# Kernel optimization log

Measured on AMD Instinct MI355X. Metric: run time of the kernel, lower is better.

The kernel has to match this reference:

```python
import jax, jax.numpy as jnp
import numpy as np

B, T, S, E, H = 4, 1024, 1024, 768, 12
D = E // H  # head_dim = 64
SCALE = D ** -0.5


def setup_inputs() -> dict:
    key = jax.random.key(0)
    ks = jax.random.split(key, 12)
    w = lambda k: jax.random.normal(k, (E, E), jnp.float32) * 0.02
    b = lambda k: jax.random.normal(k, (E,), jnp.float32) * 0.02
    return {
        "hidden_states": jax.random.normal(ks[0], (B, T, E), jnp.float32),
        "key_value_states": jax.random.normal(ks[1], (B, S, E), jnp.float32),
        "position_bias": jax.random.normal(ks[2], (T, S, D), jnp.float32),
        "Wq": w(ks[3]), "bq": b(ks[4]),
        "Wk": w(ks[5]), "bk": b(ks[6]),
        "Wv": w(ks[7]), "bv": b(ks[8]),
        "Wo": w(ks[9]), "bo": b(ks[10]),
    }


def _heads(x, L):
    # [B, L, E] -> [B, H, L, D]
    return x.reshape(B, L, H, D).transpose(0, 2, 1, 3)


def reference(hidden_states, key_value_states, position_bias,
              Wq, bq, Wk, bk, Wv, bv, Wo, bo):
    # projections (torch Linear: x @ W.T + b); query pre-scaled like original
    q = _heads((hidden_states @ Wq.T + bq) * SCALE, T)   # [B,H,T,D]
    k = _heads(key_value_states @ Wk.T + bk, S)           # [B,H,S,D]
    v = _heads(key_value_states @ Wv.T + bv, S)           # [B,H,S,D]

    # QK^T plus relative position bias (reshape_q @ position_bias^T in torch)
    scores = jnp.einsum('bhtd,bhsd->bhts', q, k)
    scores = scores + jnp.einsum('bhtd,tsd->bhts', q, position_bias)

    probs = jax.nn.softmax(scores, axis=-1)               # [B,H,T,S]
    out = jnp.einsum('bhts,bhsd->bhtd', probs, v)          # [B,H,T,D]
    out = out.transpose(0, 2, 1, 3).reshape(B, T, E)       # [B,T,E]
    return out @ Wo.T + bo
```

## Files before the change

### kernel.cpp

```cpp
#include <hip/hip_runtime.h>
#include <hip/hip_bf16.h>

#define BB 4
#define TT 1024
#define SS 1024
#define EE 768
#define HH 12
#define DD 64
#define BH (BB*HH)
#define QSCALE 0.125f

typedef __attribute__((ext_vector_type(8))) short bf16x8;
typedef __attribute__((ext_vector_type(4))) float f32x4;

__device__ __forceinline__ unsigned short bf16_rne(float x) {
    unsigned u = __builtin_bit_cast(unsigned, x);
    u += 0x7FFFu + ((u >> 16) & 1u);
    return (unsigned short)(u >> 16);
}
__device__ __forceinline__ void split_bf16(float x, unsigned short& h, unsigned short& l) {
    unsigned u = __builtin_bit_cast(unsigned, x);
    unsigned r = u + 0x7FFFu + ((u >> 16) & 1u);
    h = (unsigned short)(r >> 16);
    const float fh = __builtin_bit_cast(float, r & 0xFFFF0000u);
    l = bf16_rne(x - fh);
}

template<int HEAD_LAYOUT>
__global__ __launch_bounds__(256) void gemm_xwt_mfma(
    const float* __restrict__ X, const float* __restrict__ W,
    const float* __restrict__ bias, float* __restrict__ out, float scale)
{
    __shared__ __align__(16) unsigned short Ah[128][40], Al[128][40];
    __shared__ __align__(16) unsigned short Bh[64][40],  Bl[64][40];

    const int bm = blockIdx.x * 128, bn = blockIdx.y * 64;
    const int tid  = threadIdx.x;
    const int wave = tid >> 6, lane = tid & 63;
    const int wr = (wave >> 1) * 64;
    const int wc = (wave & 1) * 32;
    const int lr = lane & 15;
    const int lg = lane >> 4;

    f32x4 acc[4][2];
    #pragma unroll
    for (int mi = 0; mi < 4; ++mi)
        #pragma unroll
        for (int nj = 0; nj < 2; ++nj) acc[mi][nj] = (f32x4){0.f, 0.f, 0.f, 0.f};

    for (int k0 = 0; k0 < 768; k0 += 32) {
        #pragma unroll
        for (int i = 0; i < 4; ++i) {
            const int f = i * 256 + tid, r = f >> 3, c = (f & 7) * 4;
            const float4 v = *(const float4*)&X[(size_t)(bm + r) * 768 + k0 + c];
            unsigned short h0,h1,h2,h3,l0,l1,l2,l3;
            split_bf16(v.x, h0, l0); split_bf16(v.y, h1, l1);
            split_bf16(v.z, h2, l2); split_bf16(v.w, h3, l3);
            *(ushort4*)&Ah[r][c] = make_ushort4(h0, h1, h2, h3);
            *(ushort4*)&Al[r][c] = make_ushort4(l0, l1, l2, l3);
        }
        #pragma unroll
        for (int i = 0; i < 2; ++i) {
            const int f = i * 256 + tid, r = f >> 3, c = (f & 7) * 4;
            const float4 v = *(const float4*)&W[(size_t)(bn + r) * 768 + k0 + c];
            unsigned short h0,h1,h2,h3,l0,l1,l2,l3;
            split_bf16(v.x, h0, l0); split_bf16(v.y, h1, l1);
            split_bf16(v.z, h2, l2); split_bf16(v.w, h3, l3);
            *(ushort4*)&Bh[r][c] = make_ushort4(h0, h1, h2, h3);
            *(ushort4*)&Bl[r][c] = make_ushort4(l0, l1, l2, l3);
        }
        __syncthreads();

        bf16x8 ah[4], al[4], bh[2], bl[2];
        #pragma unroll
        for (int mi = 0; mi < 4; ++mi) {
            ah[mi] = *(const bf16x8*)&Ah[wr + mi * 16 + lr][lg * 8];
            al[mi] = *(const bf16x8*)&Al[wr + mi * 16 + lr][lg * 8];
        }
        #pragma unroll
        for (int nj = 0; nj < 2; ++nj) {
            bh[nj] = *(const bf16x8*)&Bh[wc + nj * 16 + lr][lg * 8];
            bl[nj] = *(const bf16x8*)&Bl[wc + nj * 16 + lr][lg * 8];
        }
        #pragma unroll
        for (int mi = 0; mi < 4; ++mi)
            #pragma unroll
            for (int nj = 0; nj < 2; ++nj) {
                acc[mi][nj] = __builtin_amdgcn_mfma_f32_16x16x32_bf16(ah[mi], bl[nj], acc[mi][nj], 0, 0, 0);
                acc[mi][nj] = __builtin_amdgcn_mfma_f32_16x16x32_bf16(al[mi], bh[nj], acc[mi][nj], 0, 0, 0);
                acc[mi][nj] = __builtin_amdgcn_mfma_f32_16x16x32_bf16(ah[mi], bh[nj], acc[mi][nj], 0, 0, 0);
            }
        __syncthreads();
    }

    #pragma unroll
    for (int mi = 0; mi < 4; ++mi) {
        #pragma unroll
        for (int nj = 0; nj < 2; ++nj) {
            const int gn = bn + wc + nj * 16 + lr;
            #pragma unroll
            for (int r = 0; r < 4; ++r) {
                const int gm = bm + wr + mi * 16 + lg * 4 + r;
                const float val = (acc[mi][nj][r] + bias[gn]) * scale;
                if (HEAD_LAYOUT) {
                    const int b = gm >> 10, l = gm & 1023;
                    const int h = gn >> 6,  d = gn & 63;
                    out[(size_t)((b * HH + h) * 1024 + l) * 64 + d] = val;
                } else {
                    out[(size_t)gm * 768 + gn] = val;
                }
            }
        }
    }
}

__global__ __launch_bounds__(192) void bias_fill(
    const float* __restrict__ q, const float* __restrict__ pos,
    float* __restrict__ biasbuf)
{
    const int t  = blockIdx.x;
    const int sc = blockIdx.y;
    __shared__ float Qs[64][49];
    __shared__ float Ps[64][129];
    const int tid = threadIdx.x;

    for (int f = tid; f < 768; f += 192) {
        const int bh = f >> 4, d4 = (f & 15) * 4;
        const float4 w = *(const float4*)&q[(size_t)(bh * 1024 + t) * 64 + d4];
        Qs[d4 + 0][bh] = w.x; Qs[d4 + 1][bh] = w.y;
        Qs[d4 + 2][bh] = w.z; Qs[d4 + 3][bh] = w.w;
    }
    for (int f = tid; f < 2048; f += 192) {
        const int sl = f >> 4, d4 = (f & 15) * 4;
        const float4 w = *(const float4*)&pos[((size_t)t * 1024 + sc * 128 + sl) * 64 + d4];
        Ps[d4 + 0][sl] = w.x; Ps[d4 + 1][sl] = w.y;
        Ps[d4 + 2][sl] = w.z; Ps[d4 + 3][sl] = w.w;
    }
    __syncthreads();

    const int sg = tid & 31;
    const int g  = tid >> 5;
    float acc[8][4];
    #pragma unroll
    for (int i = 0; i < 8; ++i)
        #pragma unroll
        for (int u = 0; u < 4; ++u) acc[i][u] = 0.f;

    #pragma unroll 4
    for (int d = 0; d < 64; ++d) {
        float p[4], qv[8];
        #pragma unroll
        for (int u = 0; u < 4; ++u) p[u] = Ps[d][sg + 32 * u];
        #pragma unroll
        for (int i = 0; i < 8; ++i) qv[i] = Qs[d][g * 8 + i];
        #pragma unroll
        for (int i = 0; i < 8; ++i)
            #pragma unroll
            for (int u = 0; u < 4; ++u) acc[i][u] += qv[i] * p[u];
    }
    #pragma unroll
    for (int i = 0; i < 8; ++i) {
        const int bh = g * 8 + i;
        #pragma unroll
        for (int u = 0; u < 4; ++u) {
            const int s = sc * 128 + sg + 32 * u;
            biasbuf[((size_t)bh * 1024 + t) * 1024 + s] = acc[i][u];
        }
    }
}

__global__ __launch_bounds__(256) void flash_attn(
    const float* __restrict__ q, const float* __restrict__ k,
    const float* __restrict__ v, const float* __restrict__ biasbuf,
    float* __restrict__ attn)
{
    const int mt = blockIdx.x;
    const int bh = blockIdx.y;
    const int b = bh / HH, h = bh % HH;
    const int tid = threadIdx.x;
    const int tx = tid & 15;
    const int ty = tid >> 4;

    __shared__ float4 Qs4[64][17];
    __shared__ float4 KP4[64][17];
    __shared__ float  Vt[64][68];

    for (int f = tid; f < 1024; f += 256) {
        const int r = f >> 4, c4 = f & 15;
        Qs4[r][c4] = *(const float4*)&q[((size_t)bh * 1024 + mt * 64 + r) * 64 + c4 * 4];
    }

    float o[4][4];
    float mrow[4], lrow[4];
    #pragma unroll
    for (int i = 0; i < 4; ++i) {
        mrow[i] = -1e30f; lrow[i] = 0.f;
        #pragma unroll
        for (int j = 0; j < 4; ++j) o[i][j] = 0.f;
    }

    for (int s0 = 0; s0 < 1024; s0 += 64) {
        float bias_r[4][4];
        #pragma unroll
        for (int i = 0; i < 4; ++i) {
            const size_t row = ((size_t)bh * 1024 + mt * 64 + ty + 16 * i) * 1024;
            #pragma unroll
            for (int j = 0; j < 4; ++j)
                bias_r[i][j] = biasbuf[row + s0 + tx + 16 * j];
        }

        __syncthreads();
        for (int f = tid; f < 1024; f += 256) {
            const int r = f >> 4, c4 = f & 15;
            KP4[r][c4] = *(const float4*)&k[((size_t)bh * 1024 + s0 + r) * 64 + c4 * 4];
        }
        for (int f = tid; f < 1024; f += 256) {
            const int r = f & 63, c4 = f >> 6;
            const float4 w = *(const float4*)&v[((size_t)bh * 1024 + s0 + r) * 64 + c4 * 4];
            Vt[c4 * 4 + 0][r] = w.x; Vt[c4 * 4 + 1][r] = w.y;
            Vt[c4 * 4 + 2][r] = w.z; Vt[c4 * 4 + 3][r] = w.w;
        }
        __syncthreads();

        float accs[4][4];
        #pragma unroll
        for (int i = 0; i < 4; ++i)
            #pragma unroll
            for (int j = 0; j < 4; ++j) accs[i][j] = bias_r[i][j];
        #pragma unroll
        for (int k4 = 0; k4 < 16; ++k4) {
            float4 a4[4], b4[4];
            #pragma unroll
            for (int i = 0; i < 4; ++i) a4[i] = Qs4[ty + 16 * i][k4];
            #pragma unroll
            for (int j = 0; j < 4; ++j) b4[j] = KP4[tx + 16 * j][k4];
            #pragma unroll
            for (int i = 0; i < 4; ++i)
                #pragma unroll
                for (int j = 0; j < 4; ++j)
                    accs[i][j] += a4[i].x * b4[j].x + a4[i].y * b4[j].y
                                + a4[i].z * b4[j].z + a4[i].w * b4[j].w;
        }

        float p[4][4];
        #pragma unroll
        for (int i = 0; i < 4; ++i) {
            float tmax = fmaxf(fmaxf(accs[i][0], accs[i][1]),
                               fmaxf(accs[i][2], accs[i][3]));
            #pragma unroll
            for (int off = 8; off > 0; off >>= 1)
                tmax = fmaxf(tmax, __shfl_xor(tmax, off, 16));
            const float newm = fmaxf(mrow[i], tmax);
            const float scale = __expf(mrow[i] - newm);
            float psum = 0.f;
            #pragma unroll
            for (int j = 0; j < 4; ++j) {
                p[i][j] = __expf(accs[i][j] - newm);
                psum += p[i][j];
            }
            #pragma unroll
            for (int off = 8; off > 0; off >>= 1)
                psum += __shfl_xor(psum, off, 16);
            lrow[i] = lrow[i] * scale + psum;
            mrow[i] = newm;
            #pragma unroll
            for (int j = 0; j < 4; ++j) o[i][j] *= scale;
        }

        __syncthreads();
        {
            float* Pf = (float*)KP4;
            #pragma unroll
            for (int i = 0; i < 4; ++i)
                #pragma unroll
                for (int j = 0; j < 4; ++j)
                    Pf[(ty + 16 * i) * 68 + tx + 16 * j] = p[i][j];
        }
        __syncthreads();

        {
            const float* Pf = (const float*)KP4;
            #pragma unroll 4
            for (int sk4 = 0; sk4 < 16; ++sk4) {
                float4 p4[4], v4[4];
                #pragma unroll
                for (int i = 0; i < 4; ++i)
                    p4[i] = *(const float4*)&Pf[(ty + 16 * i) * 68 + sk4 * 4];
                #pragma unroll
                for (int j = 0; j < 4; ++j)
                    v4[j] = *(const float4*)&Vt[tx + 16 * j][sk4 * 4];
                #pragma unroll
                for (int i = 0; i < 4; ++i)
                    #pragma unroll
                    for (int j = 0; j < 4; ++j)
                        o[i][j] += p4[i].x * v4[j].x + p4[i].y * v4[j].y
                                 + p4[i].z * v4[j].z + p4[i].w * v4[j].w;
            }
        }
    }

    #pragma unroll
    for (int i = 0; i < 4; ++i) {
        const int t = mt * 64 + ty + 16 * i;
        const float inv = 1.0f / lrow[i];
        #pragma unroll
        for (int j = 0; j < 4; ++j) {
            const int d = tx + 16 * j;
            attn[((size_t)b * 1024 + t) * 768 + h * 64 + d] = o[i][j] * inv;
        }
    }
}

extern "C" void kernel_launch(void* const* d_in, const int* in_sizes, int n_in,
                              void* d_out, int out_size, void* d_ws, size_t ws_size,
                              hipStream_t stream)
{
    const float* hidden = (const float*)d_in[0];
    const float* kv     = (const float*)d_in[1];
    const float* pos    = (const float*)d_in[2];
    const float* Wq = (const float*)d_in[3];  const float* bq = (const float*)d_in[4];
    const float* Wk = (const float*)d_in[5];  const float* bk = (const float*)d_in[6];
    const float* Wv = (const float*)d_in[7];  const float* bv = (const float*)d_in[8];
    const float* Wo = (const float*)d_in[9];  const float* bo = (const float*)d_in[10];
    float* out = (float*)d_out;

    float* q       = (float*)d_ws;
    float* kbuf    = q     + (size_t)BH * 1024 * 64;
    float* vbuf    = kbuf  + (size_t)BH * 1024 * 64;
    float* attn    = vbuf  + (size_t)BH * 1024 * 64;
    float* biasbuf = attn  + (size_t)BB * 1024 * EE;

    const dim3 gproj(32, 12), blk(256);
    gemm_xwt_mfma<1><<<gproj, blk, 0, stream>>>(hidden, Wq, bq, q,    QSCALE);
    gemm_xwt_mfma<1><<<gproj, blk, 0, stream>>>(kv,     Wk, bk, kbuf, 1.0f);
    gemm_xwt_mfma<1><<<gproj, blk, 0, stream>>>(kv,     Wv, bv, vbuf, 1.0f);

    bias_fill <<<dim3(1024, 8), 192, 0, stream>>>(q, pos, biasbuf);
    flash_attn<<<dim3(16, 48),  256, 0, stream>>>(q, kbuf, vbuf, biasbuf, attn);

    gemm_xwt_mfma<0><<<gproj, blk, 0, stream>>>(attn, Wo, bo, out, 1.0f);
}
```

Measured before the change: 912.7 us.

## Port flash attention to bf16 MFMA with split-precision QK and block swizzle

Rewrites the attention kernel so QK^T and PV run on MFMA 16x16x32 bf16 instructions instead of scalar FP32 FMAs. QK^T keeps near-FP32 accuracy by splitting Q and K into high and low bf16 parts and issuing three MFMAs, while P and V are rounded to plain bf16. Bias tiles are staged through shared memory with coalesced loads, and block IDs are remapped across a 1D grid to change scheduling and cache locality. The cost is lower precision in the PV product and extra conversion work when staging K and V.

```diff
diff --git a/kernel.cpp b/kernel.cpp
--- a/kernel.cpp
+++ b/kernel.cpp
@@ -169,144 +169,138 @@
     }
 }
 
-__global__ __launch_bounds__(256) void flash_attn(
+__global__ __launch_bounds__(256) void flash_attn_mfma(
     const float* __restrict__ q, const float* __restrict__ k,
     const float* __restrict__ v, const float* __restrict__ biasbuf,
     float* __restrict__ attn)
 {
-    const int mt = blockIdx.x;
-    const int bh = blockIdx.y;
+    __shared__ __align__(16) unsigned short Kh[64][72], Kl[64][72];
+    __shared__ __align__(16) unsigned short Vt[64][72], Pm[64][72];
+    __shared__ __align__(16) float BiasT[64][64];
+
+    const int bid = blockIdx.x;
+    const int vid = (bid & 7) * 96 + (bid >> 3);
+    const int mt = vid & 15;
+    const int bh = vid >> 4;
     const int b = bh / HH, h = bh % HH;
     const int tid = threadIdx.x;
-    const int tx = tid & 15;
-    const int ty = tid >> 4;
-
-    __shared__ float4 Qs4[64][17];
-    __shared__ float4 KP4[64][17];
-    __shared__ float  Vt[64][68];
-
-    for (int f = tid; f < 1024; f += 256) {
-        const int r = f >> 4, c4 = f & 15;
-        Qs4[r][c4] = *(const float4*)&q[((size_t)bh * 1024 + mt * 64 + r) * 64 + c4 * 4];
-    }
-
-    float o[4][4];
+    const int wave = tid >> 6, lane = tid & 63;
+    const int lr = lane & 15, lg = lane >> 4;
+    const int trow = wave * 16;
+
+    bf16x8 qh[2], ql[2];
+    {
+        const size_t qbase = ((size_t)bh * 1024 + mt * 64 + trow + lr) * 64;
+        #pragma unroll
+        for (int kst = 0; kst < 2; ++kst) {
+            const float4 x0 = *(const float4*)&q[qbase + kst * 32 + lg * 8];
+            const float4 x1 = *(const float4*)&q[qbase + kst * 32 + lg * 8 + 4];
+            const float xs[8] = {x0.x, x0.y, x0.z, x0.w, x1.x, x1.y, x1.z, x1.w};
+            #pragma unroll
+            for (int j = 0; j < 8; ++j) {
+                unsigned short hh, ll; split_bf16(xs[j], hh, ll);
+                qh[kst][j] = (short)hh; ql[kst][j] = (short)ll;
+            }
+        }
+    }
+
+    f32x4 o[4];
     float mrow[4], lrow[4];
     #pragma unroll
-    for (int i = 0; i < 4; ++i) {
-        mrow[i] = -1e30f; lrow[i] = 0.f;
-        #pragma unroll
-        for (int j = 0; j < 4; ++j) o[i][j] = 0.f;
-    }
+    for (int r = 0; r < 4; ++r) { mrow[r] = -1e30f; lrow[r] = 0.f; }
+    #pragma unroll
+    for (int nj = 0; nj < 4; ++nj) o[nj] = (f32x4){0.f, 0.f, 0.f, 0.f};
 
     for (int s0 = 0; s0 < 1024; s0 += 64) {
-        float bias_r[4][4];
+        __syncthreads();
         #pragma unroll
         for (int i = 0; i < 4; ++i) {
-            const size_t row = ((size_t)bh * 1024 + mt * 64 + ty + 16 * i) * 1024;
-            #pragma unroll
-            for (int j = 0; j < 4; ++j)
-                bias_r[i][j] = biasbuf[row + s0 + tx + 16 * j];
-        }
-
+            const int idx = i * 256 + tid;
+            const int row = idx >> 4, c = (idx & 15) * 4;
+            const float4 kk = *(const float4*)&k[((size_t)bh * 1024 + s0 + row) * 64 + c];
+            unsigned short h0,h1,h2,h3,l0,l1,l2,l3;
+            split_bf16(kk.x, h0, l0); split_bf16(kk.y, h1, l1);
+            split_bf16(kk.z, h2, l2); split_bf16(kk.w, h3, l3);
+            *(ushort4*)&Kh[row][c] = make_ushort4(h0, h1, h2, h3);
+            *(ushort4*)&Kl[row][c] = make_ushort4(l0, l1, l2, l3);
+            const float4 vv = *(const float4*)&v[((size_t)bh * 1024 + s0 + row) * 64 + c];
+            Vt[c + 0][row] = bf16_rne(vv.x); Vt[c + 1][row] = bf16_rne(vv.y);
+            Vt[c + 2][row] = bf16_rne(vv.z); Vt[c + 3][row] = bf16_rne(vv.w);
+            *(float4*)&BiasT[row][c] =
+                *(const float4*)&biasbuf[((size_t)bh * 1024 + mt * 64 + row) * 1024 + s0 + c];
+        }
         __syncthreads();
-        for (int f = tid; f < 1024; f += 256) {
-            const int r = f >> 4, c4 = f & 15;
-            KP4[r][c4] = *(const float4*)&k[((size_t)bh * 1024 + s0 + r) * 64 + c4 * 4];
-        }
-        for (int f = tid; f < 1024; f += 256) {
-            const int r = f & 63, c4 = f >> 6;
-            const float4 w = *(const float4*)&v[((size_t)bh * 1024 + s0 + r) * 64 + c4 * 4];
-            Vt[c4 * 4 + 0][r] = w.x; Vt[c4 * 4 + 1][r] = w.y;
-            Vt[c4 * 4 + 2][r] = w.z; Vt[c4 * 4 + 3][r] = w.w;
-        }
-        __syncthreads();
-
-        float accs[4][4];
-        #pragma unroll
-        for (int i = 0; i < 4; ++i)
-            #pragma unroll
-            for (int j = 0; j < 4; ++j) accs[i][j] = bias_r[i][j];
-        #pragma unroll
-        for (int k4 = 0; k4 < 16; ++k4) {
-            float4 a4[4], b4[4];
-            #pragma unroll
-            for (int i = 0; i < 4; ++i) a4[i] = Qs4[ty + 16 * i][k4];
-            #pragma unroll
-            for (int j = 0; j < 4; ++j) b4[j] = KP4[tx + 16 * j][k4];
-            #pragma unroll
-            for (int i = 0; i < 4; ++i)
-                #pragma unroll
-                for (int j = 0; j < 4; ++j)
-                    accs[i][j] += a4[i].x * b4[j].x + a4[i].y * b4[j].y
-                                + a4[i].z * b4[j].z + a4[i].w * b4[j].w;
-        }
-
-        float p[4][4];
-        #pragma unroll
-        for (int i = 0; i < 4; ++i) {
-            float tmax = fmaxf(fmaxf(accs[i][0], accs[i][1]),
-                               fmaxf(accs[i][2], accs[i][3]));
+
+        f32x4 s_acc[4];
+        #pragma unroll
+        for (int nj = 0; nj < 4; ++nj) {
+            #pragma unroll
+            for (int r = 0; r < 4; ++r)
+                s_acc[nj][r] = BiasT[trow + lg * 4 + r][nj * 16 + lr];
+            #pragma unroll
+            for (int kst = 0; kst < 2; ++kst) {
+                const bf16x8 kh = *(const bf16x8*)&Kh[nj * 16 + lr][kst * 32 + lg * 8];
+                const bf16x8 kl = *(const bf16x8*)&Kl[nj * 16 + lr][kst * 32 + lg * 8];
+                s_acc[nj] = __builtin_amdgcn_mfma_f32_16x16x32_bf16(qh[kst], kl, s_acc[nj], 0, 0, 0);
+                s_acc[nj] = __builtin_amdgcn_mfma_f32_16x16x32_bf16(ql[kst], kh, s_acc[nj], 0, 0, 0);
+                s_acc[nj] = __builtin_amdgcn_mfma_f32_16x16x32_bf16(qh[kst], kh, s_acc[nj], 0, 0, 0);
+            }
+        }
+
+        float pv[4][4];
+        #pragma unroll
+        for (int r = 0; r < 4; ++r) {
+            float tmax = fmaxf(fmaxf(s_acc[0][r], s_acc[1][r]),
+                               fmaxf(s_acc[2][r], s_acc[3][r]));
             #pragma unroll
             for (int off = 8; off > 0; off >>= 1)
                 tmax = fmaxf(tmax, __shfl_xor(tmax, off, 16));
-            const float newm = fmaxf(mrow[i], tmax);
-            const float scale = __expf(mrow[i] - newm);
+            const float newm = fmaxf(mrow[r], tmax);
+            const float rescale = __expf(mrow[r] - newm);
             float psum = 0.f;
             #pragma unroll
-            for (int j = 0; j < 4; ++j) {
-                p[i][j] = __expf(accs[i][j] - newm);
-                psum += p[i][j];
+            for (int nj = 0; nj < 4; ++nj) {
+                pv[nj][r] = __expf(s_acc[nj][r] - newm);
+                psum += pv[nj][r];
             }
             #pragma unroll
             for (int off = 8; off > 0; off >>= 1)
                 psum += __shfl_xor(psum, off, 16);
-            lrow[i] = lrow[i] * scale + psum;
-            mrow[i] = newm;
-            #pragma unroll
-            for (int j = 0; j < 4; ++j) o[i][j] *= scale;
-        }
-
-        __syncthreads();
-        {
-            float* Pf = (float*)KP4;
-            #pragma unroll
-            for (int i = 0; i < 4; ++i)
-                #pragma unroll
-                for (int j = 0; j < 4; ++j)
-                    Pf[(ty + 16 * i) * 68 + tx + 16 * j] = p[i][j];
-        }
-        __syncthreads();
-
-        {
-            const float* Pf = (const float*)KP4;
-            #pragma unroll 4
-            for (int sk4 = 0; sk4 < 16; ++sk4) {
-                float4 p4[4], v4[4];
-                #pragma unroll
-                for (int i = 0; i < 4; ++i)
-                    p4[i] = *(const float4*)&Pf[(ty + 16 * i) * 68 + sk4 * 4];
-                #pragma unroll
-                for (int j = 0; j < 4; ++j)
-                    v4[j] = *(const float4*)&Vt[tx + 16 * j][sk4 * 4];
-                #pragma unroll
-                for (int i = 0; i < 4; ++i)
-                    #pragma unroll
-                    for (int j = 0; j < 4; ++j)
-                        o[i][j] += p4[i].x * v4[j].x + p4[i].y * v4[j].y
-                                 + p4[i].z * v4[j].z + p4[i].w * v4[j].w;
-            }
-        }
-    }
-
-    #pragma unroll
-    for (int i = 0; i < 4; ++i) {
-        const int t = mt * 64 + ty + 16 * i;
-        const float inv = 1.0f / lrow[i];
-        #pragma unroll
-        for (int j = 0; j < 4; ++j) {
-            const int d = tx + 16 * j;
-            attn[((size_t)b * 1024 + t) * 768 + h * 64 + d] = o[i][j] * inv;
+            lrow[r] = lrow[r] * rescale + psum;
+            mrow[r] = newm;
+            #pragma unroll
+            for (int nj = 0; nj < 4; ++nj) o[nj][r] *= rescale;
+        }
+
+        #pragma unroll
+        for (int nj = 0; nj < 4; ++nj)
+            #pragma unroll
+            for (int r = 0; r < 4; ++r)
+                Pm[trow + lg * 4 + r][nj * 16 + lr] = bf16_rne(pv[nj][r]);
+        asm volatile("s_waitcnt lgkmcnt(0)" ::: "memory");
+        __builtin_amdgcn_sched_barrier(0);
+
+        bf16x8 pa[2];
+        pa[0] = *(const bf16x8*)&Pm[trow + lr][lg * 8];
+        pa[1] = *(const bf16x8*)&Pm[trow + lr][32 + lg * 8];
+        #pragma unroll
+        for (int nj = 0; nj < 4; ++nj) {
+            #pragma unroll
+            for (int kst = 0; kst < 2; ++kst) {
+                const bf16x8 vb = *(const bf16x8*)&Vt[nj * 16 + lr][kst * 32 + lg * 8];
+                o[nj] = __builtin_amdgcn_mfma_f32_16x16x32_bf16(pa[kst], vb, o[nj], 0, 0, 0);
+            }
+        }
+    }
+
+    #pragma unroll
+    for (int r = 0; r < 4; ++r) {
+        const int t = mt * 64 + trow + lg * 4 + r;
+        const float inv = 1.0f / lrow[r];
+        #pragma unroll
+        for (int nj = 0; nj < 4; ++nj) {
+            const int d = nj * 16 + lr;
+            attn[((size_t)b * 1024 + t) * 768 + h * 64 + d] = o[nj][r] * inv;
         }
     }
 }
@@ -335,8 +329,8 @@
     gemm_xwt_mfma<1><<<gproj, blk, 0, stream>>>(kv,     Wk, bk, kbuf, 1.0f);
     gemm_xwt_mfma<1><<<gproj, blk, 0, stream>>>(kv,     Wv, bv, vbuf, 1.0f);
 
-    bias_fill <<<dim3(1024, 8), 192, 0, stream>>>(q, pos, biasbuf);
-    flash_attn<<<dim3(16, 48),  256, 0, stream>>>(q, kbuf, vbuf, biasbuf, attn);
+    bias_fill      <<<dim3(1024, 8), 192, 0, stream>>>(q, pos, biasbuf);
+    flash_attn_mfma<<<768,           256, 0, stream>>>(q, kbuf, vbuf, biasbuf, attn);
 
     gemm_xwt_mfma<0><<<gproj, blk, 0, stream>>>(attn, Wo, bo, out, 1.0f);
 }
```

Result: faster. 800.7 us (-12.3%).
